# Kernel tuning notes

Measured on AMD Instinct MI355X. Metric: run time of the kernel, lower is better.

Reference implementation:

```python
import jax, jax.numpy as jnp
import numpy as np

B, C, M, N = 8, 64, 256, 256
THRESHOLD = 0.8
EPS = 1e-5
PAD = 3  # kernel_size=7


def conv2d(x, w, b=None):
    # x: (B,Cin,H,W), w: (Cout,Cin,7,7), stride 1, 'same' padding 3
    y = jax.lax.conv_general_dilated(
        x, w, window_strides=(1, 1), padding=[(PAD, PAD), (PAD, PAD)],
        dimension_numbers=('NCHW', 'OIHW', 'NCHW'))
    if b is not None:
        y = y + b[None, :, None, None]
    return y


def region_norm(region, mask):
    # region: (B,C,M,N) zeroed outside region; mask: (B,C,M,N) binary
    s = jnp.sum(region, axis=(0, 2, 3))            # (C,)
    Sr = jnp.sum(mask, axis=(0, 2, 3))             # (C,)
    Sr = jnp.where(Sr == 0, 1.0, Sr)
    mu = (s / Sr)[None, :, None, None]
    t = region + (1.0 - mask) * mu                 # fill surroundings with region mean
    # BatchNorm2d(affine=False, track_running_stats=False): batch stats, biased var
    m = jnp.mean(t, axis=(0, 2, 3), keepdims=True)
    v = jnp.mean((t - m) ** 2, axis=(0, 2, 3), keepdims=True)
    bn = (t - m) * jax.lax.rsqrt(v + EPS)
    scale = jnp.sqrt(Sr / (region.shape[0] * region.shape[2] * region.shape[3]))
    return bn * scale[None, :, None, None]


def setup_inputs() -> dict:
    key = jax.random.key(0)
    k = jax.random.split(key, 6)
    x = jax.random.normal(k[0], (B, C, M, N), dtype=jnp.float32)
    # conv1: Conv2d(2,1,7,bias=False); gamma/beta: Conv2d(1,1,7) with bias
    w1 = jax.random.normal(k[1], (1, 2, 7, 7), dtype=jnp.float32) * 0.1
    wg = jax.random.normal(k[2], (1, 1, 7, 7), dtype=jnp.float32) * 0.1
    bg = jax.random.normal(k[3], (1,), dtype=jnp.float32) * 0.1
    wb = jax.random.normal(k[4], (1, 1, 7, 7), dtype=jnp.float32) * 0.1
    bb = jax.random.normal(k[5], (1,), dtype=jnp.float32) * 0.1
    return {"x": x, "w1": w1, "wg": wg, "bg": bg, "wb": wb, "bb": bb}


def reference(x, w1, wg, bg, wb, bb):
    # SelfAware_Affine
    avg_out = jnp.mean(x, axis=1, keepdims=True)       # (B,1,M,N)
    max_out = jnp.max(x, axis=1, keepdims=True)        # (B,1,M,N)
    sa_in = jnp.concatenate([avg_out, max_out], axis=1)
    sa_map = jax.nn.sigmoid(conv2d(sa_in, w1))         # (B,1,M,N)
    gamma = conv2d(sa_map, wg, bg)                     # (B,1,M,N)
    beta = conv2d(sa_map, wb, bb)                      # (B,1,M,N)
    # binary mask from detached importance map, expanded over channels
    mask = (jax.lax.stop_gradient(sa_map) >= THRESHOLD).astype(x.dtype)
    mask = jnp.broadcast_to(mask, x.shape)             # (B,C,M,N)
    rn_x = region_norm(x * mask, mask) + region_norm(x * (1.0 - mask), 1.0 - mask)
    return rn_x * (1.0 + gamma) + beta
```

## Files before the change

kernel.cpp:

```cpp
#include <hip/hip_runtime.h>
#include <cmath>

#define B_ 8
#define C_ 64
#define M_ 256
#define N_ 256
#define PLANE_ (M_*N_)
#define PIX_ (B_*PLANE_)
#define THRESH_ 0.8f
#define EPS_ 1e-5f

__global__ void k_avgmax(const float* __restrict__ x,
                         float* __restrict__ avgp, float* __restrict__ maxp) {
    int idx4 = (blockIdx.x * blockDim.x + threadIdx.x) * 4;
    int b = idx4 >> 16;
    int p = idx4 & (PLANE_ - 1);
    const float* xb = x + (size_t)b * C_ * PLANE_ + p;
    float4 s = make_float4(0.f, 0.f, 0.f, 0.f);
    float4 mx = make_float4(-INFINITY, -INFINITY, -INFINITY, -INFINITY);
    #pragma unroll 8
    for (int c = 0; c < C_; ++c) {
        float4 v = *(const float4*)(xb + (size_t)c * PLANE_);
        s.x += v.x; s.y += v.y; s.z += v.z; s.w += v.w;
        mx.x = fmaxf(mx.x, v.x); mx.y = fmaxf(mx.y, v.y);
        mx.z = fmaxf(mx.z, v.z); mx.w = fmaxf(mx.w, v.w);
    }
    const float r = 1.f / C_;
    s.x *= r; s.y *= r; s.z *= r; s.w *= r;
    *(float4*)(avgp + idx4) = s;
    *(float4*)(maxp + idx4) = mx;
}

__global__ void k_saconv(const float* __restrict__ avgp, const float* __restrict__ maxp,
                         const float* __restrict__ w1, float* __restrict__ samap) {
    __shared__ float w[98];
    if (threadIdx.x < 98) w[threadIdx.x] = w1[threadIdx.x];
    __syncthreads();
    int idx = blockIdx.x * blockDim.x + threadIdx.x;
    int b = idx >> 16;
    int r = idx & (PLANE_ - 1);
    int i = r >> 8;
    int j = r & (N_ - 1);
    const float* a = avgp + (size_t)b * PLANE_;
    const float* m = maxp + (size_t)b * PLANE_;
    float acc = 0.f;
    #pragma unroll
    for (int dh = 0; dh < 7; ++dh) {
        int ii = i + dh - 3;
        if ((unsigned)ii >= (unsigned)M_) continue;
        #pragma unroll
        for (int dw = 0; dw < 7; ++dw) {
            int jj = j + dw - 3;
            if ((unsigned)jj >= (unsigned)N_) continue;
            int o = ii * N_ + jj;
            acc += a[o] * w[dh * 7 + dw] + m[o] * w[49 + dh * 7 + dw];
        }
    }
    samap[idx] = 1.f / (1.f + expf(-acc));
}

__global__ void k_gammabeta(const float* __restrict__ samap,
                            const float* __restrict__ wg, const float* __restrict__ bgp,
                            const float* __restrict__ wb, const float* __restrict__ bbp,
                            float* __restrict__ gammap, float* __restrict__ betap,
                            unsigned char* __restrict__ maskp, int* __restrict__ cntp) {
    __shared__ float w[98];
    if (threadIdx.x < 49) w[threadIdx.x] = wg[threadIdx.x];
    else if (threadIdx.x < 98) w[threadIdx.x] = wb[threadIdx.x - 49];
    __syncthreads();
    int idx = blockIdx.x * blockDim.x + threadIdx.x;
    int b = idx >> 16;
    int r = idx & (PLANE_ - 1);
    int i = r >> 8;
    int j = r & (N_ - 1);
    const float* s = samap + (size_t)b * PLANE_;
    float g = 0.f, be = 0.f;
    #pragma unroll
    for (int dh = 0; dh < 7; ++dh) {
        int ii = i + dh - 3;
        if ((unsigned)ii >= (unsigned)M_) continue;
        #pragma unroll
        for (int dw = 0; dw < 7; ++dw) {
            int jj = j + dw - 3;
            if ((unsigned)jj >= (unsigned)N_) continue;
            float v = s[ii * N_ + jj];
            g  += v * w[dh * 7 + dw];
            be += v * w[49 + dh * 7 + dw];
        }
    }
    gammap[idx] = g + bgp[0];
    betap[idx]  = be + bbp[0];
    int mk = (samap[idx] >= THRESH_) ? 1 : 0;
    maskp[idx] = (unsigned char)mk;
    unsigned long long bal = __ballot(mk);
    __shared__ int wcnt[4];
    int wave = threadIdx.x >> 6, lane = threadIdx.x & 63;
    if (lane == 0) wcnt[wave] = __popcll(bal);
    __syncthreads();
    if (threadIdx.x == 0) {
        atomicAdd(cntp, wcnt[0] + wcnt[1] + wcnt[2] + wcnt[3]);
    }
}

__global__ void k_sums(const float* __restrict__ x, const unsigned char* __restrict__ maskp,
                       float* __restrict__ S, float* __restrict__ Q,
                       float* __restrict__ S1, float* __restrict__ Q1) {
    int chunk = blockIdx.x;
    int c = blockIdx.y;
    int b = blockIdx.z;
    const float* xp = x + ((size_t)(b * C_ + c)) * PLANE_ + chunk * 8192;
    const unsigned char* mp = maskp + (size_t)b * PLANE_ + chunk * 8192;
    float s = 0.f, q = 0.f, s1 = 0.f, q1 = 0.f;
    #pragma unroll
    for (int k = 0; k < 8; ++k) {
        int t = (k * 256 + threadIdx.x) * 4;
        float4 v = *(const float4*)(xp + t);
        uchar4 mm = *(const uchar4*)(mp + t);
        float m0 = (float)mm.x, m1 = (float)mm.y, m2 = (float)mm.z, m3 = (float)mm.w;
        s  += v.x + v.y + v.z + v.w;
        q  += v.x * v.x + v.y * v.y + v.z * v.z + v.w * v.w;
        s1 += v.x * m0 + v.y * m1 + v.z * m2 + v.w * m3;
        q1 += v.x * v.x * m0 + v.y * v.y * m1 + v.z * v.z * m2 + v.w * v.w * m3;
    }
    for (int off = 32; off > 0; off >>= 1) {
        s  += __shfl_down(s, off, 64);
        q  += __shfl_down(q, off, 64);
        s1 += __shfl_down(s1, off, 64);
        q1 += __shfl_down(q1, off, 64);
    }
    __shared__ float ls[4][4];
    int wave = threadIdx.x >> 6, lane = threadIdx.x & 63;
    if (lane == 0) { ls[wave][0] = s; ls[wave][1] = q; ls[wave][2] = s1; ls[wave][3] = q1; }
    __syncthreads();
    if (threadIdx.x == 0) {
        float ts = 0.f, tq = 0.f, ts1 = 0.f, tq1 = 0.f;
        #pragma unroll
        for (int wv = 0; wv < 4; ++wv) { ts += ls[wv][0]; tq += ls[wv][1]; ts1 += ls[wv][2]; tq1 += ls[wv][3]; }
        atomicAdd(&S[c], ts); atomicAdd(&Q[c], tq);
        atomicAdd(&S1[c], ts1); atomicAdd(&Q1[c], tq1);
    }
}

__global__ void k_coef(const float* __restrict__ S, const float* __restrict__ Q,
                       const float* __restrict__ S1, const float* __restrict__ Q1,
                       const int* __restrict__ cntp,
                       float* __restrict__ cMa, float* __restrict__ cMb,
                       float* __restrict__ cUa, float* __restrict__ cUb) {
    int c = threadIdx.x;
    if (c >= C_) return;
    const float P = (float)PIX_;
    int cnt1 = *cntp;
    float fc1 = (float)cnt1;
    float fc0 = P - fc1;
    float Sr1 = (cnt1 == 0) ? 1.f : fc1;
    float Sr0 = (cnt1 == PIX_) ? 1.f : fc0;
    float Sv = S[c], Qv = Q[c], S1v = S1[c], Q1v = Q1[c];
    float S0v = Sv - S1v, Q0v = Qv - Q1v;
    float mu1 = S1v / Sr1;
    float mu0 = S0v / Sr0;
    float m1 = (S1v + fc0 * mu1) / P;
    float v1 = fmaxf((Q1v + fc0 * mu1 * mu1) / P - m1 * m1, 0.f);
    float m0 = (S0v + fc1 * mu0) / P;
    float v0 = fmaxf((Q0v + fc1 * mu0 * mu0) / P - m0 * m0, 0.f);
    float A1 = rsqrtf(v1 + EPS_) * sqrtf(Sr1 / P);
    float A0 = rsqrtf(v0 + EPS_) * sqrtf(Sr0 / P);
    float B1 = (mu1 - m1) * A1;
    float B0 = (mu0 - m0) * A0;
    cMa[c] = A1;             cMb[c] = -m1 * A1 + B0;
    cUa[c] = A0;             cUb[c] = -m0 * A0 + B1;
}

__global__ void k_final(const float* __restrict__ x, const unsigned char* __restrict__ maskp,
                        const float* __restrict__ gammap, const float* __restrict__ betap,
                        const float* __restrict__ cMa, const float* __restrict__ cMb,
                        const float* __restrict__ cUa, const float* __restrict__ cUb,
                        float* __restrict__ out) {
    int c = blockIdx.y;
    int b = blockIdx.z;
    int p0 = blockIdx.x * 1024 + threadIdx.x * 4;
    size_t base = ((size_t)(b * C_ + c)) * PLANE_ + p0;
    int pp = b * PLANE_ + p0;
    float4 xv = *(const float4*)(x + base);
    float4 gv = *(const float4*)(gammap + pp);
    float4 bv = *(const float4*)(betap + pp);
    uchar4 mv = *(const uchar4*)(maskp + pp);
    float ma = cMa[c], mb = cMb[c], ua = cUa[c], ub = cUb[c];
    float4 o;
    o.x = (mv.x ? xv.x * ma + mb : xv.x * ua + ub) * (1.f + gv.x) + bv.x;
    o.y = (mv.y ? xv.y * ma + mb : xv.y * ua + ub) * (1.f + gv.y) + bv.y;
    o.z = (mv.z ? xv.z * ma + mb : xv.z * ua + ub) * (1.f + gv.z) + bv.z;
    o.w = (mv.w ? xv.w * ma + mb : xv.w * ua + ub) * (1.f + gv.w) + bv.w;
    *(float4*)(out + base) = o;
}

extern "C" void kernel_launch(void* const* d_in, const int* in_sizes, int n_in,
                              void* d_out, int out_size, void* d_ws, size_t ws_size,
                              hipStream_t stream) {
    const float* x  = (const float*)d_in[0];
    const float* w1 = (const float*)d_in[1];
    const float* wg = (const float*)d_in[2];
    const float* bg = (const float*)d_in[3];
    const float* wb = (const float*)d_in[4];
    const float* bb = (const float*)d_in[5];
    float* out = (float*)d_out;

    float* ws = (float*)d_ws;
    float* avgp   = ws;
    float* maxp   = avgp + PIX_;
    float* samap  = maxp + PIX_;
    float* gammap = samap + PIX_;
    float* betap  = gammap + PIX_;
    float* S   = betap + PIX_;
    float* Q   = S + C_;
    float* S1  = Q + C_;
    float* Q1  = S1 + C_;
    int*   cnt = (int*)(Q1 + C_);
    float* cMa = (float*)(cnt + 1);
    float* cMb = cMa + C_;
    float* cUa = cMb + C_;
    float* cUb = cUa + C_;
    unsigned char* maskp = (unsigned char*)(cUb + C_);

    hipMemsetAsync(S, 0, (4 * C_ + 1) * sizeof(float), stream);

    k_avgmax<<<PIX_ / (256 * 4), 256, 0, stream>>>(x, avgp, maxp);
    k_saconv<<<PIX_ / 256, 256, 0, stream>>>(avgp, maxp, w1, samap);
    k_gammabeta<<<PIX_ / 256, 256, 0, stream>>>(samap, wg, bg, wb, bb,
                                                gammap, betap, maskp, cnt);
    dim3 g3(8, C_, B_);
    k_sums<<<g3, 256, 0, stream>>>(x, maskp, S, Q, S1, Q1);
    k_coef<<<1, 64, 0, stream>>>(S, Q, S1, Q1, cnt, cMa, cMb, cUa, cUb);
    dim3 g5(PLANE_ / 1024, C_, B_);
    k_final<<<g5, 256, 0, stream>>>(x, maskp, gammap, betap, cMa, cMb, cUa, cUb, out);
}
```

Measured before the change: 347.4 us.

## Fuse SA conv with gamma/beta conv via shared-memory tiles, fold coef into final

Merges the sigmoid-attention 7x7 conv and the gamma/beta 7x7 convs into one tiled kernel. It stages avg/max planes with a 6-pixel halo in LDS and recomputes the sa_map halo, so the samap buffer is no longer written to or read back from global memory. The memset is replaced by zeroing the accumulators inside the first kernel. The per-channel coefficient kernel is removed, and every k_final block now recomputes its coefficients from the sums. This cuts launches and global traffic, in exchange for redundant halo conv work and per-block scalar math.

```diff
diff --git a/kernel.cpp b/kernel.cpp
--- a/kernel.cpp
+++ b/kernel.cpp
@@ -11,7 +11,12 @@
 #define EPS_ 1e-5f
 
 __global__ void k_avgmax(const float* __restrict__ x,
-                         float* __restrict__ avgp, float* __restrict__ maxp) {
+                         float* __restrict__ avgp, float* __restrict__ maxp,
+                         float* __restrict__ acc) {
+    if (blockIdx.x == 0) {
+        if (threadIdx.x < 4 * C_) acc[threadIdx.x] = 0.f;
+        if (threadIdx.x == 0) acc[4 * C_] = 0.f;
+    }
     int idx4 = (blockIdx.x * blockDim.x + threadIdx.x) * 4;
     int b = idx4 >> 16;
     int p = idx4 & (PLANE_ - 1);
@@ -31,75 +36,95 @@
     *(float4*)(maxp + idx4) = mx;
 }
 
-__global__ void k_saconv(const float* __restrict__ avgp, const float* __restrict__ maxp,
-                         const float* __restrict__ w1, float* __restrict__ samap) {
-    __shared__ float w[98];
-    if (threadIdx.x < 98) w[threadIdx.x] = w1[threadIdx.x];
-    __syncthreads();
-    int idx = blockIdx.x * blockDim.x + threadIdx.x;
-    int b = idx >> 16;
-    int r = idx & (PLANE_ - 1);
-    int i = r >> 8;
-    int j = r & (N_ - 1);
+#define TW_ 64
+#define TH_ 16
+#define SAW_ (TW_+6)
+#define SAH_ (TH_+6)
+#define LDW_ (TW_+12)
+#define LDH_ (TH_+12)
+
+__global__ void k_sa_fused(const float* __restrict__ avgp, const float* __restrict__ maxp,
+                           const float* __restrict__ w1,
+                           const float* __restrict__ wg, const float* __restrict__ bgp,
+                           const float* __restrict__ wb, const float* __restrict__ bbp,
+                           float* __restrict__ gammap, float* __restrict__ betap,
+                           unsigned char* __restrict__ maskp, int* __restrict__ cntp) {
+    __shared__ float sA[LDH_][LDW_];
+    __shared__ float sM[LDH_][LDW_];
+    __shared__ float sSA[SAH_][SAW_];
+    __shared__ float w[196];
+    __shared__ int bcnt;
+    int tid = threadIdx.x;
+    if (tid < 98) w[tid] = w1[tid];
+    else if (tid < 196) w[tid] = (tid < 147) ? wg[tid - 98] : wb[tid - 147];
+    if (tid == 196) bcnt = 0;
+
+    int tileid = blockIdx.x;
+    int b = blockIdx.y;
+    int ti0 = (tileid >> 2) * TH_;
+    int tj0 = (tileid & 3) * TW_;
     const float* a = avgp + (size_t)b * PLANE_;
     const float* m = maxp + (size_t)b * PLANE_;
-    float acc = 0.f;
+
+    for (int idx = tid; idx < LDH_ * LDW_; idx += 256) {
+        int li = idx / LDW_;
+        int lj = idx - li * LDW_;
+        int gi = ti0 - 6 + li, gj = tj0 - 6 + lj;
+        bool ok = ((unsigned)gi < (unsigned)M_) && ((unsigned)gj < (unsigned)N_);
+        int o = gi * N_ + gj;
+        sA[li][lj] = ok ? a[o] : 0.f;
+        sM[li][lj] = ok ? m[o] : 0.f;
+    }
+    __syncthreads();
+
+    for (int idx = tid; idx < SAH_ * SAW_; idx += 256) {
+        int si = idx / SAW_;
+        int sj = idx - si * SAW_;
+        int gi = ti0 - 3 + si, gj = tj0 - 3 + sj;
+        float v = 0.f;
+        if ((unsigned)gi < (unsigned)M_ && (unsigned)gj < (unsigned)N_) {
+            float acc = 0.f;
+            #pragma unroll
+            for (int dh = 0; dh < 7; ++dh) {
+                #pragma unroll
+                for (int dw = 0; dw < 7; ++dw) {
+                    acc += sA[si + dh][sj + dw] * w[dh * 7 + dw]
+                         + sM[si + dh][sj + dw] * w[49 + dh * 7 + dw];
+                }
+            }
+            v = 1.f / (1.f + expf(-acc));
+        }
+        sSA[si][sj] = v;
+    }
+    __syncthreads();
+
+    float bgv = bgp[0], bbv = bbp[0];
+    int lcnt = 0;
     #pragma unroll
-    for (int dh = 0; dh < 7; ++dh) {
-        int ii = i + dh - 3;
-        if ((unsigned)ii >= (unsigned)M_) continue;
+    for (int k = 0; k < 4; ++k) {
+        int p = k * 256 + tid;
+        int ti = p >> 6, tj = p & 63;
+        float g = 0.f, be = 0.f;
         #pragma unroll
-        for (int dw = 0; dw < 7; ++dw) {
-            int jj = j + dw - 3;
-            if ((unsigned)jj >= (unsigned)N_) continue;
-            int o = ii * N_ + jj;
-            acc += a[o] * w[dh * 7 + dw] + m[o] * w[49 + dh * 7 + dw];
+        for (int dh = 0; dh < 7; ++dh) {
+            #pragma unroll
+            for (int dw = 0; dw < 7; ++dw) {
+                float v = sSA[ti + dh][tj + dw];
+                g  += v * w[98 + dh * 7 + dw];
+                be += v * w[147 + dh * 7 + dw];
+            }
         }
-    }
-    samap[idx] = 1.f / (1.f + expf(-acc));
-}
-
-__global__ void k_gammabeta(const float* __restrict__ samap,
-                            const float* __restrict__ wg, const float* __restrict__ bgp,
-                            const float* __restrict__ wb, const float* __restrict__ bbp,
-                            float* __restrict__ gammap, float* __restrict__ betap,
-                            unsigned char* __restrict__ maskp, int* __restrict__ cntp) {
-    __shared__ float w[98];
-    if (threadIdx.x < 49) w[threadIdx.x] = wg[threadIdx.x];
-    else if (threadIdx.x < 98) w[threadIdx.x] = wb[threadIdx.x - 49];
-    __syncthreads();
-    int idx = blockIdx.x * blockDim.x + threadIdx.x;
-    int b = idx >> 16;
-    int r = idx & (PLANE_ - 1);
-    int i = r >> 8;
-    int j = r & (N_ - 1);
-    const float* s = samap + (size_t)b * PLANE_;
-    float g = 0.f, be = 0.f;
-    #pragma unroll
-    for (int dh = 0; dh < 7; ++dh) {
-        int ii = i + dh - 3;
-        if ((unsigned)ii >= (unsigned)M_) continue;
-        #pragma unroll
-        for (int dw = 0; dw < 7; ++dw) {
-            int jj = j + dw - 3;
-            if ((unsigned)jj >= (unsigned)N_) continue;
-            float v = s[ii * N_ + jj];
-            g  += v * w[dh * 7 + dw];
-            be += v * w[49 + dh * 7 + dw];
-        }
-    }
-    gammap[idx] = g + bgp[0];
-    betap[idx]  = be + bbp[0];
-    int mk = (samap[idx] >= THRESH_) ? 1 : 0;
-    maskp[idx] = (unsigned char)mk;
-    unsigned long long bal = __ballot(mk);
-    __shared__ int wcnt[4];
-    int wave = threadIdx.x >> 6, lane = threadIdx.x & 63;
-    if (lane == 0) wcnt[wave] = __popcll(bal);
-    __syncthreads();
-    if (threadIdx.x == 0) {
-        atomicAdd(cntp, wcnt[0] + wcnt[1] + wcnt[2] + wcnt[3]);
-    }
+        int idx = b * PLANE_ + (ti0 + ti) * N_ + (tj0 + tj);
+        gammap[idx] = g + bgv;
+        betap[idx]  = be + bbv;
+        int mk = (sSA[ti + 3][tj + 3] >= THRESH_) ? 1 : 0;
+        maskp[idx] = (unsigned char)mk;
+        lcnt += mk;
+    }
+    for (int off = 32; off > 0; off >>= 1) lcnt += __shfl_down(lcnt, off, 64);
+    if ((tid & 63) == 0) atomicAdd(&bcnt, lcnt);
+    __syncthreads();
+    if (tid == 0) atomicAdd(cntp, bcnt);
 }
 
 __global__ void k_sums(const float* __restrict__ x, const unsigned char* __restrict__ maskp,
@@ -141,13 +166,14 @@
     }
 }
 
-__global__ void k_coef(const float* __restrict__ S, const float* __restrict__ Q,
-                       const float* __restrict__ S1, const float* __restrict__ Q1,
-                       const int* __restrict__ cntp,
-                       float* __restrict__ cMa, float* __restrict__ cMb,
-                       float* __restrict__ cUa, float* __restrict__ cUb) {
-    int c = threadIdx.x;
-    if (c >= C_) return;
+__global__ void k_final(const float* __restrict__ x, const unsigned char* __restrict__ maskp,
+                        const float* __restrict__ gammap, const float* __restrict__ betap,
+                        const float* __restrict__ S, const float* __restrict__ Q,
+                        const float* __restrict__ S1, const float* __restrict__ Q1,
+                        const int* __restrict__ cntp,
+                        float* __restrict__ out) {
+    int c = blockIdx.y;
+    int b = blockIdx.z;
     const float P = (float)PIX_;
     int cnt1 = *cntp;
     float fc1 = (float)cnt1;
@@ -166,17 +192,9 @@
     float A0 = rsqrtf(v0 + EPS_) * sqrtf(Sr0 / P);
     float B1 = (mu1 - m1) * A1;
     float B0 = (mu0 - m0) * A0;
-    cMa[c] = A1;             cMb[c] = -m1 * A1 + B0;
-    cUa[c] = A0;             cUb[c] = -m0 * A0 + B1;
-}
-
-__global__ void k_final(const float* __restrict__ x, const unsigned char* __restrict__ maskp,
-                        const float* __restrict__ gammap, const float* __restrict__ betap,
-                        const float* __restrict__ cMa, const float* __restrict__ cMb,
-                        const float* __restrict__ cUa, const float* __restrict__ cUb,
-                        float* __restrict__ out) {
-    int c = blockIdx.y;
-    int b = blockIdx.z;
+    float ma = A1, mb = -m1 * A1 + B0;
+    float ua = A0, ub = -m0 * A0 + B1;
+
     int p0 = blockIdx.x * 1024 + threadIdx.x * 4;
     size_t base = ((size_t)(b * C_ + c)) * PLANE_ + p0;
     int pp = b * PLANE_ + p0;
@@ -184,7 +202,6 @@
     float4 gv = *(const float4*)(gammap + pp);
     float4 bv = *(const float4*)(betap + pp);
     uchar4 mv = *(const uchar4*)(maskp + pp);
-    float ma = cMa[c], mb = cMb[c], ua = cUa[c], ub = cUb[c];
     float4 o;
     o.x = (mv.x ? xv.x * ma + mb : xv.x * ua + ub) * (1.f + gv.x) + bv.x;
     o.y = (mv.y ? xv.y * ma + mb : xv.y * ua + ub) * (1.f + gv.y) + bv.y;
@@ -207,29 +224,21 @@
     float* ws = (float*)d_ws;
     float* avgp   = ws;
     float* maxp   = avgp + PIX_;
-    float* samap  = maxp + PIX_;
-    float* gammap = samap + PIX_;
+    float* gammap = maxp + PIX_;
     float* betap  = gammap + PIX_;
     float* S   = betap + PIX_;
     float* Q   = S + C_;
     float* S1  = Q + C_;
     float* Q1  = S1 + C_;
     int*   cnt = (int*)(Q1 + C_);
-    float* cMa = (float*)(cnt + 1);
-    float* cMb = cMa + C_;
-    float* cUa = cMb + C_;
-    float* cUb = cUa + C_;
-    unsigned char* maskp = (unsigned char*)(cUb + C_);
-
-    hipMemsetAsync(S, 0, (4 * C_ + 1) * sizeof(float), stream);
-
-    k_avgmax<<<PIX_ / (256 * 4), 256, 0, stream>>>(x, avgp, maxp);
-    k_saconv<<<PIX_ / 256, 256, 0, stream>>>(avgp, maxp, w1, samap);
-    k_gammabeta<<<PIX_ / 256, 256, 0, stream>>>(samap, wg, bg, wb, bb,
-                                                gammap, betap, maskp, cnt);
+    unsigned char* maskp = (unsigned char*)(cnt + 1);
+
+    k_avgmax<<<PIX_ / (256 * 4), 256, 0, stream>>>(x, avgp, maxp, S);
+    dim3 g2(64, B_);
+    k_sa_fused<<<g2, 256, 0, stream>>>(avgp, maxp, w1, wg, bg, wb, bb,
+                                       gammap, betap, maskp, cnt);
     dim3 g3(8, C_, B_);
     k_sums<<<g3, 256, 0, stream>>>(x, maskp, S, Q, S1, Q1);
-    k_coef<<<1, 64, 0, stream>>>(S, Q, S1, Q1, cnt, cMa, cMb, cUa, cUb);
     dim3 g5(PLANE_ / 1024, C_, B_);
-    k_final<<<g5, 256, 0, stream>>>(x, maskp, gammap, betap, cMa, cMb, cUa, cUb, out);
-}
+    k_final<<<g5, 256, 0, stream>>>(x, maskp, gammap, betap, S, Q, S1, Q1, cnt, out);
+}
```

Measured after the change: 335.5 us. 3.4% less time.
